# Performance work log

Measured on AMD Instinct MI355X. Metric: run time of the kernel, lower is better.

## Reference

```python
import jax, jax.numpy as jnp
import numpy as np

B, N = 8, 2048
IN_F, MID1, HID, MID2, OUT_F = 128, 128, 128, 128, 128
BIG = 9e15  # matches torch's 9000000000000000.0 additive mask constant


def _linear_params(key, out_d, in_d):
    # torch Linear layout: W is [out, in]
    kw, kb = jax.random.split(key)
    w = jax.random.normal(kw, (out_d, in_d), jnp.float32) * (1.0 / np.sqrt(in_d))
    b = jax.random.normal(kb, (out_d,), jnp.float32) * 0.01
    return w, b


def setup_inputs() -> dict:
    key = jax.random.key(0)
    ks = jax.random.split(key, 16)
    h = jax.random.normal(ks[0], (B, N, IN_F), jnp.float32)
    adj = jax.random.randint(ks[1], (B, N, N), 0, 2).astype(jnp.float32)
    vae2_fetures = jax.random.normal(ks[2], (B, N, OUT_F), jnp.float32)
    Wv1, bv1 = _linear_params(ks[3], MID1, IN_F)
    Wk1, bk1 = _linear_params(ks[4], MID1, IN_F)
    Wq1, bq1 = _linear_params(ks[5], MID1, IN_F)
    Wo1, bo1 = _linear_params(ks[6], HID, MID1)
    Wv2, bv2 = _linear_params(ks[7], MID2, HID)
    Wk2, bk2 = _linear_params(ks[8], MID2, HID)
    Wq2, bq2 = _linear_params(ks[9], MID2, HID)
    Wo2, bo2 = _linear_params(ks[10], OUT_F, MID2)
    Wf, bf = _linear_params(ks[11], OUT_F, 2 * OUT_F)
    return {
        "h": h, "adj": adj, "vae2_fetures": vae2_fetures,
        "Wv1": Wv1, "bv1": bv1, "Wk1": Wk1, "bk1": bk1, "Wq1": Wq1, "bq1": bq1,
        "Wo1": Wo1, "bo1": bo1,
        "Wv2": Wv2, "bv2": bv2, "Wk2": Wk2, "bk2": bk2, "Wq2": Wq2, "bq2": bq2,
        "Wo2": Wo2, "bo2": bo2, "Wf": Wf, "bf": bf,
    }


def _lin(x, W, b):
    return jnp.einsum('bnd,od->bno', x, W) + b


def _masked_att_block(x, adj, Wq, bq, Wk, bk, Wv, bv):
    v = jax.nn.relu(_lin(x, Wv, bv))          # [B,N,D]
    q = jax.nn.relu(_lin(x, Wq, bq))          # [B,N,D]
    k = jax.nn.relu(_lin(x, Wk, bk))          # [B,N,D]
    s = jnp.einsum('bnd,bmd->bnm', q, k)       # [B,N,N]
    masked = s * adj - BIG * (1.0 - adj)       # multiplicative + additive mask
    att = jax.nn.softmax(masked, axis=-1)
    return jnp.einsum('bnm,bmd->bnd', att, v)


def reference(h, adj, vae2_fetures,
              Wv1, bv1, Wk1, bk1, Wq1, bq1, Wo1, bo1,
              Wv2, bv2, Wk2, bk2, Wq2, bq2, Wo2, bo2,
              Wf, bf):
    f1 = _masked_att_block(h, adj, Wq1, bq1, Wk1, bk1, Wv1, bv1)
    f1 = _lin(f1, Wo1, bo1)                    # [B,N,HID]
    f2 = _masked_att_block(f1, adj, Wq2, bq2, Wk2, bk2, Wv2, bv2)
    f2 = _lin(f2, Wo2, bo2)                    # [B,N,OUT_F]
    f3 = jnp.concatenate([f2, vae2_fetures], axis=2)
    return _lin(f3, Wf, bf)                    # [B,N,OUT_F]
```

## Files before the change

kernel.cpp:

```cpp
#include <hip/hip_runtime.h>

typedef short s16x8 __attribute__((ext_vector_type(8)));
typedef float f32x4 __attribute__((ext_vector_type(4)));
typedef unsigned short u16x4v __attribute__((ext_vector_type(4)));

#define NSPLIT 4
#define NROWS 16384
#define MSHIFT 44.0f
#define NCH (2048 / NSPLIT / 64)

__device__ __forceinline__ unsigned short f2bf(float f) {
  union { float fl; unsigned int i; } v; v.fl = f;
  unsigned int x = v.i;
  x += 0x7fffu + ((x >> 16) & 1u);
  return (unsigned short)(x >> 16);
}
__device__ __forceinline__ s16x8 load8_bf16(const unsigned short* p) {
  return *(const s16x8*)p;
}
__device__ __forceinline__ s16x8 load8_f32(const float* p) {
  float4 a = *(const float4*)p;
  float4 b = *(const float4*)(p + 4);
  s16x8 r;
  r[0] = (short)f2bf(a.x); r[1] = (short)f2bf(a.y);
  r[2] = (short)f2bf(a.z); r[3] = (short)f2bf(a.w);
  r[4] = (short)f2bf(b.x); r[5] = (short)f2bf(b.y);
  r[6] = (short)f2bf(b.z); r[7] = (short)f2bf(b.w);
  return r;
}
__device__ __forceinline__ int vperm(int nn) {
  return (nn & ~31) | (((nn >> 2) & 3) << 3) | (((nn >> 4) & 1) << 2);
}

__device__ __forceinline__ void gload16(const void* g, void* l) {
  __builtin_amdgcn_global_load_lds(
      (const __attribute__((address_space(1))) void*)g,
      (__attribute__((address_space(3))) void*)l, 16, 0, 0);
}

__device__ __forceinline__ void pack_adj_body(
    const float* __restrict__ ADJ, unsigned long long* __restrict__ MASK,
    int pblk)
{
  const int t = threadIdx.x;
  const int w = t >> 6;
  const int lane = t & 63;
  const int row = pblk * 4 + w;

  const float4* src = (const float4*)(ADJ + (size_t)row * 2048);
  float4 v[8];
#pragma unroll
  for (int j = 0; j < 8; ++j) v[j] = src[j * 64 + lane];

  unsigned long long wm = 0ull;
#pragma unroll
  for (int j = 0; j < 8; ++j) {
    const unsigned long long b0 = __ballot(v[j].x != 0.f);
    wm = (lane == j * 4 + 0) ? b0 : wm;
    const unsigned long long b1 = __ballot(v[j].y != 0.f);
    wm = (lane == j * 4 + 1) ? b1 : wm;
    const unsigned long long b2 = __ballot(v[j].z != 0.f);
    wm = (lane == j * 4 + 2) ? b2 : wm;
    const unsigned long long b3 = __ballot(v[j].w != 0.f);
    wm = (lane == j * 4 + 3) ? b3 : wm;
  }

  if (lane < 32) MASK[(size_t)row * 32 + lane] = wm;
}

__device__ __forceinline__ void qkv_merged_body(
    const float* __restrict__ X,
    const float* __restrict__ Wq, const float* __restrict__ bq, unsigned short* __restrict__ oq,
    const float* __restrict__ Wk, const float* __restrict__ bk, unsigned short* __restrict__ ok,
    const float* __restrict__ Wv, const float* __restrict__ bv, unsigned short* __restrict__ ovt)
{
  const int t = threadIdx.x;
  const int w = t >> 6;
  const int lane = t & 63;
  const int l15 = lane & 15;
  const int quad = lane >> 4;
  const int mbase = blockIdx.x * 64;

  s16x8 af[4][4];
#pragma unroll
  for (int mt = 0; mt < 4; ++mt) {
    const float* ar = X + (size_t)(mbase + mt * 16 + l15) * 128;
#pragma unroll
    for (int ks = 0; ks < 4; ++ks) af[mt][ks] = load8_f32(ar + ks * 32 + quad * 8);
  }

  const float* Ws[3] = {Wq, Wk, Wv};
  const float* bs[3] = {bq, bk, bv};
  unsigned short* outs[3] = {oq, ok, ovt};

#pragma unroll
  for (int which = 0; which < 3; ++which) {
    const float* W = Ws[which];
    const float* bias = bs[which];
    unsigned short* out = outs[which];
#pragma unroll
    for (int nt = 0; nt < 2; ++nt) {
      const int n = (w * 2 + nt) * 16 + l15;
      const float* wr = W + (size_t)n * 128;
      s16x8 wf[4];
#pragma unroll
      for (int ks = 0; ks < 4; ++ks) wf[ks] = load8_f32(wr + ks * 32 + quad * 8);
      f32x4 acc[4];
#pragma unroll
      for (int mt = 0; mt < 4; ++mt) acc[mt] = (f32x4){0.f, 0.f, 0.f, 0.f};
#pragma unroll
      for (int mt = 0; mt < 4; ++mt)
#pragma unroll
        for (int ks = 0; ks < 4; ++ks)
          acc[mt] = __builtin_amdgcn_mfma_f32_16x16x32_bf16(af[mt][ks], wf[ks], acc[mt], 0, 0, 0);
      const float bv_ = bias[n];
      if (which < 2) {
#pragma unroll
        for (int mt = 0; mt < 4; ++mt)
#pragma unroll
          for (int r = 0; r < 4; ++r)
            out[(size_t)(mbase + mt * 16 + quad * 4 + r) * 128 + n] =
                f2bf(fmaxf(acc[mt][r] + bv_, 0.f));
      } else {
        const int b = mbase >> 11;
#pragma unroll
        for (int mt = 0; mt < 4; ++mt) {
          const int nn = (mbase & 2047) + mt * 16 + quad * 4;
          u16x4v pk;
#pragma unroll
          for (int r = 0; r < 4; ++r) pk[r] = f2bf(fmaxf(acc[mt][r] + bv_, 0.f));
          *(u16x4v*)(out + (size_t)(b * 128 + n) * 2048 + vperm(nn)) = pk;
        }
      }
    }
  }
}

__global__ __launch_bounds__(256) void qkv1_kernel(
    const float* __restrict__ x,
    const float* __restrict__ Wq, const float* __restrict__ bq, unsigned short* __restrict__ oq,
    const float* __restrict__ Wk, const float* __restrict__ bk, unsigned short* __restrict__ ok,
    const float* __restrict__ Wv, const float* __restrict__ bv, unsigned short* __restrict__ ovt,
    const float* __restrict__ adj, unsigned long long* __restrict__ mask)
{
  if (blockIdx.x < 256) qkv_merged_body(x, Wq, bq, oq, Wk, bk, ok, Wv, bv, ovt);
  else                  pack_adj_body(adj, mask, blockIdx.x - 256);
}

__global__ __launch_bounds__(256, 2) void attn_kernel(
    const unsigned short* __restrict__ Q,
    const unsigned short* __restrict__ K,
    const unsigned short* __restrict__ VT,
    const unsigned long long* __restrict__ MASK,
    float* __restrict__ pO, float* __restrict__ pl)
{
  __shared__ __align__(16) unsigned short kbuf[2][64][128];
  __shared__ __align__(16) unsigned short vbuf[2][128][64];

  const int t = threadIdx.x;
  const int w = t >> 6;
  const int lane = t & 63;
  const int l15 = lane & 15;
  const int quad = lane >> 4;
  const int x7 = l15 & 7;

  const int gq0 = blockIdx.x * 128;
  const int b   = gq0 >> 11;
  const int wq0 = (gq0 & 2047) + w * 32;
  const int kc0 = blockIdx.y * (2048 / NSPLIT);

  const unsigned short* Kb  = K  + (size_t)(b * 2048) * 128;
  const unsigned short* VTb = VT + (size_t)(b * 128) * 2048;
  const unsigned long long* Mb = MASK + (size_t)b * 2048 * 32;

  const int krow = t >> 4;
  const int kc16 = t & 15;
  const int kchunk = kc16 ^ (krow & 7);
  const int vrow = t >> 3;
  const int vc16 = t & 7;
  const int vchunk = vc16 ^ (vrow & 7);

  s16x8 qf[2][4];
#pragma unroll
  for (int mt = 0; mt < 2; ++mt) {
    const unsigned short* qrow = Q + (size_t)(gq0 + w * 32 + mt * 16 + l15) * 128;
#pragma unroll
    for (int ks = 0; ks < 4; ++ks) qf[mt][ks] = load8_bf16(qrow + ks * 32 + quad * 8);
  }

  s16x8 ones;
#pragma unroll
  for (int i = 0; i < 8; ++i) ones[i] = (short)0x3F80;

  f32x4 accO[2][8];
  f32x4 accL[2];
#pragma unroll
  for (int mt = 0; mt < 2; ++mt) {
    accL[mt] = (f32x4){0.f, 0.f, 0.f, 0.f};
#pragma unroll
    for (int dt = 0; dt < 8; ++dt) accO[mt][dt] = (f32x4){0.f, 0.f, 0.f, 0.f};
  }

#pragma unroll
  for (int i = 0; i < 4; ++i)
    gload16(Kb + (size_t)(kc0 + i * 16 + krow) * 128 + kchunk * 8,
            &kbuf[0][i * 16 + krow][kc16 * 8]);
#pragma unroll
  for (int i = 0; i < 4; ++i)
    gload16(VTb + (size_t)(i * 32 + vrow) * 2048 + kc0 + vchunk * 8,
            &vbuf[0][i * 32 + vrow][vc16 * 8]);

  __syncthreads();

  for (int g = 0; g < 2; ++g) {
    const int jj = (kc0 >> 8) + g;
    ulonglong2 m01[2], m23[2];
#pragma unroll
    for (int mt = 0; mt < 2; ++mt) {
      const unsigned long long* mrow = Mb + (size_t)(wq0 + mt * 16 + l15) * 32 + jj * 4;
      m01[mt] = *(const ulonglong2*)mrow;
      m23[mt] = *(const ulonglong2*)(mrow + 2);
    }

#pragma unroll
    for (int cg = 0; cg < 4; ++cg) {
      const int kc = kc0 + g * 256 + cg * 64;
      unsigned short (*kb)[128] = kbuf[cg & 1];
      unsigned short (*vb)[64]  = vbuf[cg & 1];

      if (g == 0 || cg < 3) {
        unsigned short (*kbn)[128] = kbuf[(cg + 1) & 1];
        unsigned short (*vbn)[64]  = vbuf[(cg + 1) & 1];
#pragma unroll
        for (int i = 0; i < 4; ++i)
          gload16(Kb + (size_t)(kc + 64 + i * 16 + krow) * 128 + kchunk * 8,
                  &kbn[i * 16 + krow][kc16 * 8]);
#pragma unroll
        for (int i = 0; i < 4; ++i)
          gload16(VTb + (size_t)(i * 32 + vrow) * 2048 + (kc + 64) + vchunk * 8,
                  &vbn[i * 32 + vrow][vc16 * 8]);
      }

      f32x4 sv[2][4];
#pragma unroll
      for (int nt = 0; nt < 4; ++nt) {
        sv[0][nt] = (f32x4){0.f, 0.f, 0.f, 0.f};
        sv[1][nt] = (f32x4){0.f, 0.f, 0.f, 0.f};
      }
      __builtin_amdgcn_s_setprio(1);
#pragma unroll
      for (int nt = 0; nt < 4; ++nt)
#pragma unroll
        for (int ks = 0; ks < 4; ++ks) {
          s16x8 kf = *(const s16x8*)&kb[nt * 16 + l15][((ks * 4 + quad) ^ x7) * 8];
          sv[0][nt] = __builtin_amdgcn_mfma_f32_16x16x32_bf16(kf, qf[0][ks], sv[0][nt], 0, 0, 0);
          sv[1][nt] = __builtin_amdgcn_mfma_f32_16x16x32_bf16(kf, qf[1][ks], sv[1][nt], 0, 0, 0);
        }
      __builtin_amdgcn_s_setprio(0);

      s16x8 pf[2][2];
#pragma unroll
      for (int mt = 0; mt < 2; ++mt) {
        const unsigned long long bse0 = m01[mt].x >> (cg * 16 + quad);
        const unsigned long long bse1 = m01[mt].y >> (cg * 16 + quad);
        const unsigned long long bse2 = m23[mt].x >> (cg * 16 + quad);
        const unsigned long long bse3 = m23[mt].y >> (cg * 16 + quad);
#pragma unroll
        for (int ks = 0; ks < 2; ++ks) {
          s16x8 v;
#pragma unroll
          for (int half = 0; half < 2; ++half) {
            const int nt = ks * 2 + half;
#pragma unroll
            for (int r = 0; r < 4; ++r) {
              const float e = __expf(sv[mt][nt][r] - MSHIFT);
              const unsigned long long bw = (r == 0) ? bse0 : (r == 1) ? bse1
                                          : (r == 2) ? bse2 : bse3;
              const bool keep = (bw >> (nt * 4)) & 1ull;
              v[half * 4 + r] = (short)f2bf(keep ? e : 0.f);
            }
          }
          pf[mt][ks] = v;
        }
      }

      __builtin_amdgcn_s_setprio(1);
#pragma unroll
      for (int mt = 0; mt < 2; ++mt)
#pragma unroll
        for (int ks = 0; ks < 2; ++ks)
          accL[mt] = __builtin_amdgcn_mfma_f32_16x16x32_bf16(ones, pf[mt][ks], accL[mt], 0, 0, 0);

#pragma unroll
      for (int dt = 0; dt < 8; ++dt)
#pragma unroll
        for (int ks = 0; ks < 2; ++ks) {
          s16x8 vf = *(const s16x8*)&vb[dt * 16 + l15][((ks * 4 + quad) ^ x7) * 8];
          accO[0][dt] = __builtin_amdgcn_mfma_f32_16x16x32_bf16(vf, pf[0][ks], accO[0][dt], 0, 0, 0);
          accO[1][dt] = __builtin_amdgcn_mfma_f32_16x16x32_bf16(vf, pf[1][ks], accO[1][dt], 0, 0, 0);
        }
      __builtin_amdgcn_s_setprio(0);

      __syncthreads();
    }
  }

  float* pOs = pO + (size_t)blockIdx.y * NROWS * 128;
#pragma unroll
  for (int mt = 0; mt < 2; ++mt) {
    const int qg = gq0 + w * 32 + mt * 16 + l15;
#pragma unroll
    for (int dt = 0; dt < 8; ++dt)
      *(f32x4*)(pOs + (size_t)qg * 128 + dt * 16 + quad * 4) = accO[mt][dt];
  }
  if (quad == 0) {
#pragma unroll
    for (int mt = 0; mt < 2; ++mt)
      pl[blockIdx.y * NROWS + gq0 + w * 32 + mt * 16 + l15] = accL[mt][0];
  }
}

__device__ __forceinline__ void combine64(
    const float* __restrict__ pO, const float* __restrict__ pl, int grow0,
    unsigned short (*At)[136])
{
  const int t = threadIdx.x;
#pragma unroll
  for (int u = 0; u < 4; ++u) {
    const int unit = u * 256 + t;
    const int row = unit >> 4;
    const int col8 = (unit & 15) * 8;
    const int grow = grow0 + row;
    float lsum = 0.f;
#pragma unroll
    for (int s = 0; s < NSPLIT; ++s) lsum += pl[s * NROWS + grow];
    const float inv = (lsum > 0.f) ? 1.f / lsum : 0.f;
    float acc8[8];
#pragma unroll
    for (int i = 0; i < 8; ++i) acc8[i] = 0.f;
#pragma unroll
    for (int s = 0; s < NSPLIT; ++s) {
      const float* p = pO + (size_t)s * NROWS * 128 + (size_t)grow * 128 + col8;
      float4 x0 = *(const float4*)p;
      float4 x1 = *(const float4*)(p + 4);
      acc8[0] += x0.x; acc8[1] += x0.y; acc8[2] += x0.z; acc8[3] += x0.w;
      acc8[4] += x1.x; acc8[5] += x1.y; acc8[6] += x1.z; acc8[7] += x1.w;
    }
#pragma unroll
    for (int i = 0; i < 8; ++i) At[row][col8 + i] = f2bf(acc8[i] * inv);
  }
}

__global__ __launch_bounds__(256) void redqkv_kernel(
    const float* __restrict__ pO, const float* __restrict__ pl,
    const float* __restrict__ Wo, const float* __restrict__ bo,
    const float* __restrict__ Wq, const float* __restrict__ bq, unsigned short* __restrict__ oq,
    const float* __restrict__ Wk, const float* __restrict__ bk, unsigned short* __restrict__ ok,
    const float* __restrict__ Wv, const float* __restrict__ bv, unsigned short* __restrict__ ovt)
{
  __shared__ __align__(16) unsigned short At[64][136];
  __shared__ __align__(16) unsigned short Bt[64][136];
  const int t = threadIdx.x;
  const int grow0 = blockIdx.x * 64;

  combine64(pO, pl, grow0, At);
  __syncthreads();

  const int w = t >> 6;
  const int lane = t & 63;
  const int l15 = lane & 15;
  const int quad = lane >> 4;

  s16x8 af[4][4];
#pragma unroll
  for (int mt = 0; mt < 4; ++mt)
#pragma unroll
    for (int ks = 0; ks < 4; ++ks)
      af[mt][ks] = *(const s16x8*)&At[mt * 16 + l15][ks * 32 + quad * 8];

#pragma unroll
  for (int nt = 0; nt < 2; ++nt) {
    const int n = (w * 2 + nt) * 16 + l15;
    const float* wr = Wo + (size_t)n * 128;
    s16x8 wf[4];
#pragma unroll
    for (int ks = 0; ks < 4; ++ks) wf[ks] = load8_f32(wr + ks * 32 + quad * 8);
    f32x4 acc[4];
#pragma unroll
    for (int mt = 0; mt < 4; ++mt) acc[mt] = (f32x4){0.f, 0.f, 0.f, 0.f};
#pragma unroll
    for (int mt = 0; mt < 4; ++mt)
#pragma unroll
      for (int ks = 0; ks < 4; ++ks)
        acc[mt] = __builtin_amdgcn_mfma_f32_16x16x32_bf16(af[mt][ks], wf[ks], acc[mt], 0, 0, 0);
    const float bv_ = bo[n];
#pragma unroll
    for (int mt = 0; mt < 4; ++mt)
#pragma unroll
      for (int r = 0; r < 4; ++r)
        Bt[mt * 16 + quad * 4 + r][n] = f2bf(acc[mt][r] + bv_);
  }
  __syncthreads();

  s16x8 a2[4][4];
#pragma unroll
  for (int mt = 0; mt < 4; ++mt)
#pragma unroll
    for (int ks = 0; ks < 4; ++ks)
      a2[mt][ks] = *(const s16x8*)&Bt[mt * 16 + l15][ks * 32 + quad * 8];

#pragma unroll
  for (int which = 0; which < 3; ++which) {
    const float* W = (which == 0) ? Wq : (which == 1) ? Wk : Wv;
    const float* bb = (which == 0) ? bq : (which == 1) ? bk : bv;
    unsigned short* out = (which == 0) ? oq : (which == 1) ? ok : ovt;
#pragma unroll
    for (int nt = 0; nt < 2; ++nt) {
      const int n = (w * 2 + nt) * 16 + l15;
      const float* wr = W + (size_t)n * 128;
      s16x8 wf[4];
#pragma unroll
      for (int ks = 0; ks < 4; ++ks) wf[ks] = load8_f32(wr + ks * 32 + quad * 8);
      f32x4 acc[4];
#pragma unroll
      for (int mt = 0; mt < 4; ++mt) acc[mt] = (f32x4){0.f, 0.f, 0.f, 0.f};
#pragma unroll
      for (int mt = 0; mt < 4; ++mt)
#pragma unroll
        for (int ks = 0; ks < 4; ++ks)
          acc[mt] = __builtin_amdgcn_mfma_f32_16x16x32_bf16(a2[mt][ks], wf[ks], acc[mt], 0, 0, 0);
      const float bv_ = bb[n];
      if (which < 2) {
#pragma unroll
        for (int mt = 0; mt < 4; ++mt)
#pragma unroll
          for (int r = 0; r < 4; ++r)
            out[(size_t)(grow0 + mt * 16 + quad * 4 + r) * 128 + n] =
                f2bf(fmaxf(acc[mt][r] + bv_, 0.f));
      } else {
        const int b = grow0 >> 11;
#pragma unroll
        for (int mt = 0; mt < 4; ++mt) {
          const int nn = (grow0 & 2047) + mt * 16 + quad * 4;
          u16x4v pk;
#pragma unroll
          for (int r = 0; r < 4; ++r) pk[r] = f2bf(fmaxf(acc[mt][r] + bv_, 0.f));
          *(u16x4v*)(out + (size_t)(b * 128 + n) * 2048 + vperm(nn)) = pk;
        }
      }
    }
  }
}

__global__ __launch_bounds__(256) void redfinal_kernel(
    const float* __restrict__ pO, const float* __restrict__ pl,
    const float* __restrict__ Wo, const float* __restrict__ bo,
    const float* __restrict__ Wf, const float* __restrict__ bff,
    const float* __restrict__ vae2, float* __restrict__ out)
{
  __shared__ __align__(16) unsigned short At[64][136];
  __shared__ __align__(16) unsigned short Bt[64][136];
  const int t = threadIdx.x;
  const int grow0 = blockIdx.x * 64;

  combine64(pO, pl, grow0, At);
  __syncthreads();

  const int w = t >> 6;
  const int lane = t & 63;
  const int l15 = lane & 15;
  const int quad = lane >> 4;

  s16x8 af[4][4];
#pragma unroll
  for (int mt = 0; mt < 4; ++mt)
#pragma unroll
    for (int ks = 0; ks < 4; ++ks)
      af[mt][ks] = *(const s16x8*)&At[mt * 16 + l15][ks * 32 + quad * 8];

#pragma unroll
  for (int nt = 0; nt < 2; ++nt) {
    const int n = (w * 2 + nt) * 16 + l15;
    const float* wr = Wo + (size_t)n * 128;
    s16x8 wf[4];
#pragma unroll
    for (int ks = 0; ks < 4; ++ks) wf[ks] = load8_f32(wr + ks * 32 + quad * 8);
    f32x4 acc[4];
#pragma unroll
    for (int mt = 0; mt < 4; ++mt) acc[mt] = (f32x4){0.f, 0.f, 0.f, 0.f};
#pragma unroll
    for (int mt = 0; mt < 4; ++mt)
#pragma unroll
      for (int ks = 0; ks < 4; ++ks)
        acc[mt] = __builtin_amdgcn_mfma_f32_16x16x32_bf16(af[mt][ks], wf[ks], acc[mt], 0, 0, 0);
    const float bv_ = bo[n];
#pragma unroll
    for (int mt = 0; mt < 4; ++mt)
#pragma unroll
      for (int r = 0; r < 4; ++r)
        Bt[mt * 16 + quad * 4 + r][n] = f2bf(acc[mt][r] + bv_);
  }
  __syncthreads();

  s16x8 a1[4][4], a2[4][4];
#pragma unroll
  for (int mt = 0; mt < 4; ++mt) {
#pragma unroll
    for (int ks = 0; ks < 4; ++ks)
      a1[mt][ks] = *(const s16x8*)&Bt[mt * 16 + l15][ks * 32 + quad * 8];
    const float* vrow = vae2 + (size_t)(grow0 + mt * 16 + l15) * 128;
#pragma unroll
    for (int ks = 0; ks < 4; ++ks) a2[mt][ks] = load8_f32(vrow + ks * 32 + quad * 8);
  }

#pragma unroll
  for (int nt = 0; nt < 2; ++nt) {
    const int n = (w * 2 + nt) * 16 + l15;
    const float* wr = Wf + (size_t)n * 256;
    s16x8 wfl[4], wfr[4];
#pragma unroll
    for (int ks = 0; ks < 4; ++ks) {
      wfl[ks] = load8_f32(wr + ks * 32 + quad * 8);
      wfr[ks] = load8_f32(wr + 128 + ks * 32 + quad * 8);
    }
    f32x4 acc[4];
#pragma unroll
    for (int mt = 0; mt < 4; ++mt) acc[mt] = (f32x4){0.f, 0.f, 0.f, 0.f};
#pragma unroll
    for (int mt = 0; mt < 4; ++mt) {
#pragma unroll
      for (int ks = 0; ks < 4; ++ks)
        acc[mt] = __builtin_amdgcn_mfma_f32_16x16x32_bf16(a1[mt][ks], wfl[ks], acc[mt], 0, 0, 0);
#pragma unroll
      for (int ks = 0; ks < 4; ++ks)
        acc[mt] = __builtin_amdgcn_mfma_f32_16x16x32_bf16(a2[mt][ks], wfr[ks], acc[mt], 0, 0, 0);
    }
    const float bv_ = bff[n];
#pragma unroll
    for (int mt = 0; mt < 4; ++mt)
#pragma unroll
      for (int r = 0; r < 4; ++r)
        out[(size_t)(grow0 + mt * 16 + quad * 4 + r) * 128 + n] = acc[mt][r] + bv_;
  }
}

extern "C" void kernel_launch(void* const* d_in, const int* in_sizes, int n_in,
                              void* d_out, int out_size, void* d_ws, size_t ws_size,
                              hipStream_t stream)
{
  const float* h    = (const float*)d_in[0];
  const float* adj  = (const float*)d_in[1];
  const float* vae2 = (const float*)d_in[2];
  const float* Wv1  = (const float*)d_in[3];
  const float* bv1  = (const float*)d_in[4];
  const float* Wk1  = (const float*)d_in[5];
  const float* bk1  = (const float*)d_in[6];
  const float* Wq1  = (const float*)d_in[7];
  const float* bq1  = (const float*)d_in[8];
  const float* Wo1  = (const float*)d_in[9];
  const float* bo1  = (const float*)d_in[10];
  const float* Wv2  = (const float*)d_in[11];
  const float* bv2  = (const float*)d_in[12];
  const float* Wk2  = (const float*)d_in[13];
  const float* bk2  = (const float*)d_in[14];
  const float* Wq2  = (const float*)d_in[15];
  const float* bq2  = (const float*)d_in[16];
  const float* Wo2  = (const float*)d_in[17];
  const float* bo2  = (const float*)d_in[18];
  const float* Wf   = (const float*)d_in[19];
  const float* bff  = (const float*)d_in[20];

  char* wsb = (char*)d_ws;
  const size_t MB = 1u << 20;
  unsigned short* s_q  = (unsigned short*)(wsb + 0 * MB);
  unsigned short* s_k  = (unsigned short*)(wsb + 4 * MB);
  unsigned short* s_vt = (unsigned short*)(wsb + 8 * MB);
  unsigned long long* maskp = (unsigned long long*)(wsb + 12 * MB);
  float* pO = (float*)(wsb + 16 * MB);
  float* pl = (float*)(wsb + 48 * MB);

  qkv1_kernel<<<dim3(256 + 4096), dim3(256), 0, stream>>>(
      h, Wq1, bq1, s_q, Wk1, bk1, s_k, Wv1, bv1, s_vt, adj, maskp);
  attn_kernel<<<dim3(128, NSPLIT), dim3(256), 0, stream>>>(
      s_q, s_k, s_vt, maskp, pO, pl);
  redqkv_kernel<<<dim3(256), dim3(256), 0, stream>>>(
      pO, pl, Wo1, bo1, Wq2, bq2, s_q, Wk2, bk2, s_k, Wv2, bv2, s_vt);
  attn_kernel<<<dim3(128, NSPLIT), dim3(256), 0, stream>>>(
      s_q, s_k, s_vt, maskp, pO, pl);
  redfinal_kernel<<<dim3(256), dim3(256), 0, stream>>>(
      pO, pl, Wo2, bo2, Wf, bff, vae2, (float*)d_out);
}
```

Measured before the change: 355.0 us.

## Fuse all stages into one cooperative persistent kernel with grid syncs

Replaces the five separate launches with a single cooperative kernel of 256 blocks of 512 threads. It uses grid-wide barriers between the QKV/mask-pack, attention, reduce+QKV, attention and final stages, and falls back to separate 512-thread kernels if the cooperative launch fails. Block work is re-tiled to 512 threads: each warp now handles one 16-column slice, attention covers 256 query rows per block, and mask packing does 64 rows per block. The aim is to remove launch gaps and tail effects between kernels. In exchange, grid.sync costs are added, occupancy is fixed by the cooperative launch, and a per-process static flag caches whether cooperative launch is supported.

```diff
diff --git a/kernel.cpp b/kernel.cpp
--- a/kernel.cpp
+++ b/kernel.cpp
@@ -1,4 +1,7 @@
 #include <hip/hip_runtime.h>
+#include <hip/hip_cooperative_groups.h>
+
+namespace cg = cooperative_groups;
 
 typedef short s16x8 __attribute__((ext_vector_type(8)));
 typedef float f32x4 __attribute__((ext_vector_type(4)));
@@ -7,7 +10,6 @@
 #define NSPLIT 4
 #define NROWS 16384
 #define MSHIFT 44.0f
-#define NCH (2048 / NSPLIT / 64)
 
 __device__ __forceinline__ unsigned short f2bf(float f) {
   union { float fl; unsigned int i; } v; v.fl = f;
@@ -38,48 +40,51 @@
       (__attribute__((address_space(3))) void*)l, 16, 0, 0);
 }
 
-__device__ __forceinline__ void pack_adj_body(
+__device__ __forceinline__ void pack64_body(
     const float* __restrict__ ADJ, unsigned long long* __restrict__ MASK,
-    int pblk)
+    int bid)
 {
   const int t = threadIdx.x;
   const int w = t >> 6;
   const int lane = t & 63;
-  const int row = pblk * 4 + w;
-
-  const float4* src = (const float4*)(ADJ + (size_t)row * 2048);
-  float4 v[8];
-#pragma unroll
-  for (int j = 0; j < 8; ++j) v[j] = src[j * 64 + lane];
-
-  unsigned long long wm = 0ull;
-#pragma unroll
-  for (int j = 0; j < 8; ++j) {
-    const unsigned long long b0 = __ballot(v[j].x != 0.f);
-    wm = (lane == j * 4 + 0) ? b0 : wm;
-    const unsigned long long b1 = __ballot(v[j].y != 0.f);
-    wm = (lane == j * 4 + 1) ? b1 : wm;
-    const unsigned long long b2 = __ballot(v[j].z != 0.f);
-    wm = (lane == j * 4 + 2) ? b2 : wm;
-    const unsigned long long b3 = __ballot(v[j].w != 0.f);
-    wm = (lane == j * 4 + 3) ? b3 : wm;
-  }
-
-  if (lane < 32) MASK[(size_t)row * 32 + lane] = wm;
-}
-
-__device__ __forceinline__ void qkv_merged_body(
+  const int row0 = bid * 64 + w * 8;
+
+  for (int i = 0; i < 8; ++i) {
+    const int row = row0 + i;
+    const float4* src = (const float4*)(ADJ + (size_t)row * 2048);
+    float4 v[8];
+#pragma unroll
+    for (int j = 0; j < 8; ++j) v[j] = src[j * 64 + lane];
+
+    unsigned long long wm = 0ull;
+#pragma unroll
+    for (int j = 0; j < 8; ++j) {
+      const unsigned long long b0 = __ballot(v[j].x != 0.f);
+      wm = (lane == j * 4 + 0) ? b0 : wm;
+      const unsigned long long b1 = __ballot(v[j].y != 0.f);
+      wm = (lane == j * 4 + 1) ? b1 : wm;
+      const unsigned long long b2 = __ballot(v[j].z != 0.f);
+      wm = (lane == j * 4 + 2) ? b2 : wm;
+      const unsigned long long b3 = __ballot(v[j].w != 0.f);
+      wm = (lane == j * 4 + 3) ? b3 : wm;
+    }
+    if (lane < 32) MASK[(size_t)row * 32 + lane] = wm;
+  }
+}
+
+__device__ __forceinline__ void qkv64_body(
     const float* __restrict__ X,
     const float* __restrict__ Wq, const float* __restrict__ bq, unsigned short* __restrict__ oq,
     const float* __restrict__ Wk, const float* __restrict__ bk, unsigned short* __restrict__ ok,
-    const float* __restrict__ Wv, const float* __restrict__ bv, unsigned short* __restrict__ ovt)
+    const float* __restrict__ Wv, const float* __restrict__ bv, unsigned short* __restrict__ ovt,
+    int bid)
 {
   const int t = threadIdx.x;
   const int w = t >> 6;
   const int lane = t & 63;
   const int l15 = lane & 15;
   const int quad = lane >> 4;
-  const int mbase = blockIdx.x * 64;
+  const int mbase = bid * 64;
 
   s16x8 af[4][4];
 #pragma unroll
@@ -92,71 +97,54 @@
   const float* Ws[3] = {Wq, Wk, Wv};
   const float* bs[3] = {bq, bk, bv};
   unsigned short* outs[3] = {oq, ok, ovt};
+  const int n = w * 16 + l15;
 
 #pragma unroll
   for (int which = 0; which < 3; ++which) {
-    const float* W = Ws[which];
-    const float* bias = bs[which];
+    const float* wr = Ws[which] + (size_t)n * 128;
+    s16x8 wf[4];
+#pragma unroll
+    for (int ks = 0; ks < 4; ++ks) wf[ks] = load8_f32(wr + ks * 32 + quad * 8);
+    f32x4 acc[4];
+#pragma unroll
+    for (int mt = 0; mt < 4; ++mt) acc[mt] = (f32x4){0.f, 0.f, 0.f, 0.f};
+#pragma unroll
+    for (int mt = 0; mt < 4; ++mt)
+#pragma unroll
+      for (int ks = 0; ks < 4; ++ks)
+        acc[mt] = __builtin_amdgcn_mfma_f32_16x16x32_bf16(af[mt][ks], wf[ks], acc[mt], 0, 0, 0);
+    const float bv_ = bs[which][n];
     unsigned short* out = outs[which];
-#pragma unroll
-    for (int nt = 0; nt < 2; ++nt) {
-      const int n = (w * 2 + nt) * 16 + l15;
-      const float* wr = W + (size_t)n * 128;
-      s16x8 wf[4];
-#pragma unroll
-      for (int ks = 0; ks < 4; ++ks) wf[ks] = load8_f32(wr + ks * 32 + quad * 8);
-      f32x4 acc[4];
-#pragma unroll
-      for (int mt = 0; mt < 4; ++mt) acc[mt] = (f32x4){0.f, 0.f, 0.f, 0.f};
+    if (which < 2) {
 #pragma unroll
       for (int mt = 0; mt < 4; ++mt)
 #pragma unroll
-        for (int ks = 0; ks < 4; ++ks)
-          acc[mt] = __builtin_amdgcn_mfma_f32_16x16x32_bf16(af[mt][ks], wf[ks], acc[mt], 0, 0, 0);
-      const float bv_ = bias[n];
-      if (which < 2) {
-#pragma unroll
-        for (int mt = 0; mt < 4; ++mt)
-#pragma unroll
-          for (int r = 0; r < 4; ++r)
-            out[(size_t)(mbase + mt * 16 + quad * 4 + r) * 128 + n] =
-                f2bf(fmaxf(acc[mt][r] + bv_, 0.f));
-      } else {
-        const int b = mbase >> 11;
-#pragma unroll
-        for (int mt = 0; mt < 4; ++mt) {
-          const int nn = (mbase & 2047) + mt * 16 + quad * 4;
-          u16x4v pk;
-#pragma unroll
-          for (int r = 0; r < 4; ++r) pk[r] = f2bf(fmaxf(acc[mt][r] + bv_, 0.f));
-          *(u16x4v*)(out + (size_t)(b * 128 + n) * 2048 + vperm(nn)) = pk;
-        }
+        for (int r = 0; r < 4; ++r)
+          out[(size_t)(mbase + mt * 16 + quad * 4 + r) * 128 + n] =
+              f2bf(fmaxf(acc[mt][r] + bv_, 0.f));
+    } else {
+      const int b = mbase >> 11;
+#pragma unroll
+      for (int mt = 0; mt < 4; ++mt) {
+        const int nn = (mbase & 2047) + mt * 16 + quad * 4;
+        u16x4v pk;
+#pragma unroll
+        for (int r = 0; r < 4; ++r) pk[r] = f2bf(fmaxf(acc[mt][r] + bv_, 0.f));
+        *(u16x4v*)(out + (size_t)(b * 128 + n) * 2048 + vperm(nn)) = pk;
       }
     }
   }
 }
 
-__global__ __launch_bounds__(256) void qkv1_kernel(
-    const float* __restrict__ x,
-    const float* __restrict__ Wq, const float* __restrict__ bq, unsigned short* __restrict__ oq,
-    const float* __restrict__ Wk, const float* __restrict__ bk, unsigned short* __restrict__ ok,
-    const float* __restrict__ Wv, const float* __restrict__ bv, unsigned short* __restrict__ ovt,
-    const float* __restrict__ adj, unsigned long long* __restrict__ mask)
-{
-  if (blockIdx.x < 256) qkv_merged_body(x, Wq, bq, oq, Wk, bk, ok, Wv, bv, ovt);
-  else                  pack_adj_body(adj, mask, blockIdx.x - 256);
-}
-
-__global__ __launch_bounds__(256, 2) void attn_kernel(
+__device__ __forceinline__ void attn_body(
     const unsigned short* __restrict__ Q,
     const unsigned short* __restrict__ K,
     const unsigned short* __restrict__ VT,
     const unsigned long long* __restrict__ MASK,
-    float* __restrict__ pO, float* __restrict__ pl)
-{
-  __shared__ __align__(16) unsigned short kbuf[2][64][128];
-  __shared__ __align__(16) unsigned short vbuf[2][128][64];
-
+    float* __restrict__ pO, float* __restrict__ pl,
+    unsigned short (*kbuf)[64][128], unsigned short (*vbuf)[128][64],
+    int qb, int sp)
+{
   const int t = threadIdx.x;
   const int w = t >> 6;
   const int lane = t & 63;
@@ -164,21 +152,17 @@
   const int quad = lane >> 4;
   const int x7 = l15 & 7;
 
-  const int gq0 = blockIdx.x * 128;
+  const int gq0 = qb * 256;
   const int b   = gq0 >> 11;
   const int wq0 = (gq0 & 2047) + w * 32;
-  const int kc0 = blockIdx.y * (2048 / NSPLIT);
+  const int kc0 = sp * (2048 / NSPLIT);
 
   const unsigned short* Kb  = K  + (size_t)(b * 2048) * 128;
   const unsigned short* VTb = VT + (size_t)(b * 128) * 2048;
   const unsigned long long* Mb = MASK + (size_t)b * 2048 * 32;
 
-  const int krow = t >> 4;
-  const int kc16 = t & 15;
-  const int kchunk = kc16 ^ (krow & 7);
-  const int vrow = t >> 3;
-  const int vc16 = t & 7;
-  const int vchunk = vc16 ^ (vrow & 7);
+  const int kchunk = (t & 15) ^ ((t >> 4) & 7);
+  const int vchunk = (t & 7) ^ ((t >> 3) & 7);
 
   s16x8 qf[2][4];
 #pragma unroll
@@ -202,13 +186,17 @@
   }
 
 #pragma unroll
-  for (int i = 0; i < 4; ++i)
-    gload16(Kb + (size_t)(kc0 + i * 16 + krow) * 128 + kchunk * 8,
-            &kbuf[0][i * 16 + krow][kc16 * 8]);
-#pragma unroll
-  for (int i = 0; i < 4; ++i)
-    gload16(VTb + (size_t)(i * 32 + vrow) * 2048 + kc0 + vchunk * 8,
-            &vbuf[0][i * 32 + vrow][vc16 * 8]);
+  for (int i = 0; i < 2; ++i) {
+    const int slot = i * 512 + t;
+    gload16(Kb + (size_t)(kc0 + (slot >> 4)) * 128 + kchunk * 8,
+            &kbuf[0][slot >> 4][(slot & 15) * 8]);
+  }
+#pragma unroll
+  for (int i = 0; i < 2; ++i) {
+    const int slot = i * 512 + t;
+    gload16(VTb + (size_t)(slot >> 3) * 2048 + kc0 + vchunk * 8,
+            &vbuf[0][slot >> 3][(slot & 7) * 8]);
+  }
 
   __syncthreads();
 
@@ -223,22 +211,26 @@
     }
 
 #pragma unroll
-    for (int cg = 0; cg < 4; ++cg) {
-      const int kc = kc0 + g * 256 + cg * 64;
-      unsigned short (*kb)[128] = kbuf[cg & 1];
-      unsigned short (*vb)[64]  = vbuf[cg & 1];
-
-      if (g == 0 || cg < 3) {
-        unsigned short (*kbn)[128] = kbuf[(cg + 1) & 1];
-        unsigned short (*vbn)[64]  = vbuf[(cg + 1) & 1];
-#pragma unroll
-        for (int i = 0; i < 4; ++i)
-          gload16(Kb + (size_t)(kc + 64 + i * 16 + krow) * 128 + kchunk * 8,
-                  &kbn[i * 16 + krow][kc16 * 8]);
-#pragma unroll
-        for (int i = 0; i < 4; ++i)
-          gload16(VTb + (size_t)(i * 32 + vrow) * 2048 + (kc + 64) + vchunk * 8,
-                  &vbn[i * 32 + vrow][vc16 * 8]);
+    for (int cgi = 0; cgi < 4; ++cgi) {
+      const int kc = kc0 + g * 256 + cgi * 64;
+      unsigned short (*kb)[128] = kbuf[cgi & 1];
+      unsigned short (*vb)[64]  = vbuf[cgi & 1];
+
+      if (g == 0 || cgi < 3) {
+        unsigned short (*kbn)[128] = kbuf[(cgi + 1) & 1];
+        unsigned short (*vbn)[64]  = vbuf[(cgi + 1) & 1];
+#pragma unroll
+        for (int i = 0; i < 2; ++i) {
+          const int slot = i * 512 + t;
+          gload16(Kb + (size_t)(kc + 64 + (slot >> 4)) * 128 + kchunk * 8,
+                  &kbn[slot >> 4][(slot & 15) * 8]);
+        }
+#pragma unroll
+        for (int i = 0; i < 2; ++i) {
+          const int slot = i * 512 + t;
+          gload16(VTb + (size_t)(slot >> 3) * 2048 + (kc + 64) + vchunk * 8,
+                  &vbn[slot >> 3][(slot & 7) * 8]);
+        }
       }
 
       f32x4 sv[2][4];
@@ -261,10 +253,10 @@
       s16x8 pf[2][2];
 #pragma unroll
       for (int mt = 0; mt < 2; ++mt) {
-        const unsigned long long bse0 = m01[mt].x >> (cg * 16 + quad);
-        const unsigned long long bse1 = m01[mt].y >> (cg * 16 + quad);
-        const unsigned long long bse2 = m23[mt].x >> (cg * 16 + quad);
-        const unsigned long long bse3 = m23[mt].y >> (cg * 16 + quad);
+        const unsigned long long bse0 = m01[mt].x >> (cgi * 16 + quad);
+        const unsigned long long bse1 = m01[mt].y >> (cgi * 16 + quad);
+        const unsigned long long bse2 = m23[mt].x >> (cgi * 16 + quad);
+        const unsigned long long bse3 = m23[mt].y >> (cgi * 16 + quad);
 #pragma unroll
         for (int ks = 0; ks < 2; ++ks) {
           s16x8 v;
@@ -305,7 +297,7 @@
     }
   }
 
-  float* pOs = pO + (size_t)blockIdx.y * NROWS * 128;
+  float* pOs = pO + (size_t)sp * NROWS * 128;
 #pragma unroll
   for (int mt = 0; mt < 2; ++mt) {
     const int qg = gq0 + w * 32 + mt * 16 + l15;
@@ -316,7 +308,7 @@
   if (quad == 0) {
 #pragma unroll
     for (int mt = 0; mt < 2; ++mt)
-      pl[blockIdx.y * NROWS + gq0 + w * 32 + mt * 16 + l15] = accL[mt][0];
+      pl[sp * NROWS + gq0 + w * 32 + mt * 16 + l15] = accL[mt][0];
   }
 }
 
@@ -326,8 +318,8 @@
 {
   const int t = threadIdx.x;
 #pragma unroll
-  for (int u = 0; u < 4; ++u) {
-    const int unit = u * 256 + t;
+  for (int u = 0; u < 2; ++u) {
+    const int unit = u * 512 + t;
     const int row = unit >> 4;
     const int col8 = (unit & 15) * 8;
     const int grow = grow0 + row;
@@ -351,7 +343,254 @@
   }
 }
 
-__global__ __launch_bounds__(256) void redqkv_kernel(
+__device__ __forceinline__ void redqkv64_body(
+    const float* __restrict__ pO, const float* __restrict__ pl,
+    const float* __restrict__ Wo, const float* __restrict__ bo,
+    const float* __restrict__ Wq, const float* __restrict__ bq, unsigned short* __restrict__ oq,
+    const float* __restrict__ Wk, const float* __restrict__ bk, unsigned short* __restrict__ ok,
+    const float* __restrict__ Wv, const float* __restrict__ bv, unsigned short* __restrict__ ovt,
+    unsigned short (*At)[136], unsigned short (*Bt)[136], int bid)
+{
+  const int t = threadIdx.x;
+  const int grow0 = bid * 64;
+
+  combine64(pO, pl, grow0, At);
+  __syncthreads();
+
+  const int w = t >> 6;
+  const int lane = t & 63;
+  const int l15 = lane & 15;
+  const int quad = lane >> 4;
+  const int n = w * 16 + l15;
+
+  s16x8 af[4][4];
+#pragma unroll
+  for (int mt = 0; mt < 4; ++mt)
+#pragma unroll
+    for (int ks = 0; ks < 4; ++ks)
+      af[mt][ks] = *(const s16x8*)&At[mt * 16 + l15][ks * 32 + quad * 8];
+
+  {
+    const float* wr = Wo + (size_t)n * 128;
+    s16x8 wf[4];
+#pragma unroll
+    for (int ks = 0; ks < 4; ++ks) wf[ks] = load8_f32(wr + ks * 32 + quad * 8);
+    f32x4 acc[4];
+#pragma unroll
+    for (int mt = 0; mt < 4; ++mt) acc[mt] = (f32x4){0.f, 0.f, 0.f, 0.f};
+#pragma unroll
+    for (int mt = 0; mt < 4; ++mt)
+#pragma unroll
+      for (int ks = 0; ks < 4; ++ks)
+        acc[mt] = __builtin_amdgcn_mfma_f32_16x16x32_bf16(af[mt][ks], wf[ks], acc[mt], 0, 0, 0);
+    const float bv_ = bo[n];
+#pragma unroll
+    for (int mt = 0; mt < 4; ++mt)
+#pragma unroll
+      for (int r = 0; r < 4; ++r)
+        Bt[mt * 16 + quad * 4 + r][n] = f2bf(acc[mt][r] + bv_);
+  }
+  __syncthreads();
+
+  s16x8 a2[4][4];
+#pragma unroll
+  for (int mt = 0; mt < 4; ++mt)
+#pragma unroll
+    for (int ks = 0; ks < 4; ++ks)
+      a2[mt][ks] = *(const s16x8*)&Bt[mt * 16 + l15][ks * 32 + quad * 8];
+
+#pragma unroll
+  for (int which = 0; which < 3; ++which) {
+    const float* W = (which == 0) ? Wq : (which == 1) ? Wk : Wv;
+    const float* bb = (which == 0) ? bq : (which == 1) ? bk : bv;
+    unsigned short* out = (which == 0) ? oq : (which == 1) ? ok : ovt;
+    const float* wr = W + (size_t)n * 128;
+    s16x8 wf[4];
+#pragma unroll
+    for (int ks = 0; ks < 4; ++ks) wf[ks] = load8_f32(wr + ks * 32 + quad * 8);
+    f32x4 acc[4];
+#pragma unroll
+    for (int mt = 0; mt < 4; ++mt) acc[mt] = (f32x4){0.f, 0.f, 0.f, 0.f};
+#pragma unroll
+    for (int mt = 0; mt < 4; ++mt)
+#pragma unroll
+      for (int ks = 0; ks < 4; ++ks)
+        acc[mt] = __builtin_amdgcn_mfma_f32_16x16x32_bf16(a2[mt][ks], wf[ks], acc[mt], 0, 0, 0);
+    const float bv_ = bb[n];
+    if (which < 2) {
+#pragma unroll
+      for (int mt = 0; mt < 4; ++mt)
+#pragma unroll
+        for (int r = 0; r < 4; ++r)
+          out[(size_t)(grow0 + mt * 16 + quad * 4 + r) * 128 + n] =
+              f2bf(fmaxf(acc[mt][r] + bv_, 0.f));
+    } else {
+      const int b = grow0 >> 11;
+#pragma unroll
+      for (int mt = 0; mt < 4; ++mt) {
+        const int nn = (grow0 & 2047) + mt * 16 + quad * 4;
+        u16x4v pk;
+#pragma unroll
+        for (int r = 0; r < 4; ++r) pk[r] = f2bf(fmaxf(acc[mt][r] + bv_, 0.f));
+        *(u16x4v*)(out + (size_t)(b * 128 + n) * 2048 + vperm(nn)) = pk;
+      }
+    }
+  }
+}
+
+__device__ __forceinline__ void redfinal64_body(
+    const float* __restrict__ pO, const float* __restrict__ pl,
+    const float* __restrict__ Wo, const float* __restrict__ bo,
+    const float* __restrict__ Wf, const float* __restrict__ bff,
+    const float* __restrict__ vae2, float* __restrict__ out,
+    unsigned short (*At)[136], unsigned short (*Bt)[136], int bid)
+{
+  const int t = threadIdx.x;
+  const int grow0 = bid * 64;
+
+  combine64(pO, pl, grow0, At);
+  __syncthreads();
+
+  const int w = t >> 6;
+  const int lane = t & 63;
+  const int l15 = lane & 15;
+  const int quad = lane >> 4;
+  const int n = w * 16 + l15;
+
+  s16x8 af[4][4];
+#pragma unroll
+  for (int mt = 0; mt < 4; ++mt)
+#pragma unroll
+    for (int ks = 0; ks < 4; ++ks)
+      af[mt][ks] = *(const s16x8*)&At[mt * 16 + l15][ks * 32 + quad * 8];
+
+  {
+    const float* wr = Wo + (size_t)n * 128;
+    s16x8 wf[4];
+#pragma unroll
+    for (int ks = 0; ks < 4; ++ks) wf[ks] = load8_f32(wr + ks * 32 + quad * 8);
+    f32x4 acc[4];
+#pragma unroll
+    for (int mt = 0; mt < 4; ++mt) acc[mt] = (f32x4){0.f, 0.f, 0.f, 0.f};
+#pragma unroll
+    for (int mt = 0; mt < 4; ++mt)
+#pragma unroll
+      for (int ks = 0; ks < 4; ++ks)
+        acc[mt] = __builtin_amdgcn_mfma_f32_16x16x32_bf16(af[mt][ks], wf[ks], acc[mt], 0, 0, 0);
+    const float bv_ = bo[n];
+#pragma unroll
+    for (int mt = 0; mt < 4; ++mt)
+#pragma unroll
+      for (int r = 0; r < 4; ++r)
+        Bt[mt * 16 + quad * 4 + r][n] = f2bf(acc[mt][r] + bv_);
+  }
+  __syncthreads();
+
+  s16x8 a1[4][4], a2[4][4];
+#pragma unroll
+  for (int mt = 0; mt < 4; ++mt) {
+#pragma unroll
+    for (int ks = 0; ks < 4; ++ks)
+      a1[mt][ks] = *(const s16x8*)&Bt[mt * 16 + l15][ks * 32 + quad * 8];
+    const float* vrow = vae2 + (size_t)(grow0 + mt * 16 + l15) * 128;
+#pragma unroll
+    for (int ks = 0; ks < 4; ++ks) a2[mt][ks] = load8_f32(vrow + ks * 32 + quad * 8);
+  }
+
+  {
+    const float* wr = Wf + (size_t)n * 256;
+    s16x8 wfl[4], wfr[4];
+#pragma unroll
+    for (int ks = 0; ks < 4; ++ks) {
+      wfl[ks] = load8_f32(wr + ks * 32 + quad * 8);
+      wfr[ks] = load8_f32(wr + 128 + ks * 32 + quad * 8);
+    }
+    f32x4 acc[4];
+#pragma unroll
+    for (int mt = 0; mt < 4; ++mt) acc[mt] = (f32x4){0.f, 0.f, 0.f, 0.f};
+#pragma unroll
+    for (int mt = 0; mt < 4; ++mt) {
+#pragma unroll
+      for (int ks = 0; ks < 4; ++ks)
+        acc[mt] = __builtin_amdgcn_mfma_f32_16x16x32_bf16(a1[mt][ks], wfl[ks], acc[mt], 0, 0, 0);
+#pragma unroll
+      for (int ks = 0; ks < 4; ++ks)
+        acc[mt] = __builtin_amdgcn_mfma_f32_16x16x32_bf16(a2[mt][ks], wfr[ks], acc[mt], 0, 0, 0);
+    }
+    const float bv_ = bff[n];
+#pragma unroll
+    for (int mt = 0; mt < 4; ++mt)
+#pragma unroll
+      for (int r = 0; r < 4; ++r)
+        out[(size_t)(grow0 + mt * 16 + quad * 4 + r) * 128 + n] = acc[mt][r] + bv_;
+  }
+}
+
+__global__ __launch_bounds__(512, 2) void fused_kernel(
+    const float* __restrict__ x, const float* __restrict__ adj, const float* __restrict__ vae2,
+    const float* __restrict__ Wq1, const float* __restrict__ bq1,
+    const float* __restrict__ Wk1, const float* __restrict__ bk1,
+    const float* __restrict__ Wv1, const float* __restrict__ bv1,
+    const float* __restrict__ Wo1, const float* __restrict__ bo1,
+    const float* __restrict__ Wq2, const float* __restrict__ bq2,
+    const float* __restrict__ Wk2, const float* __restrict__ bk2,
+    const float* __restrict__ Wv2, const float* __restrict__ bv2,
+    const float* __restrict__ Wo2, const float* __restrict__ bo2,
+    const float* __restrict__ Wf, const float* __restrict__ bff,
+    unsigned short* __restrict__ s_q, unsigned short* __restrict__ s_k,
+    unsigned short* __restrict__ s_vt, unsigned long long* __restrict__ maskp,
+    float* __restrict__ pO, float* __restrict__ pl, float* __restrict__ out)
+{
+  __shared__ __align__(16) unsigned char smem[65536];
+  unsigned short (*kbuf)[64][128] = (unsigned short (*)[64][128])smem;
+  unsigned short (*vbuf)[128][64] = (unsigned short (*)[128][64])(smem + 32768);
+  unsigned short (*At)[136] = (unsigned short (*)[136])smem;
+  unsigned short (*Bt)[136] = (unsigned short (*)[136])(smem + 32768);
+
+  const int bid = blockIdx.x;
+  const int qb = bid & 63;
+  const int sp = bid >> 6;
+  cg::grid_group grid = cg::this_grid();
+
+  qkv64_body(x, Wq1, bq1, s_q, Wk1, bk1, s_k, Wv1, bv1, s_vt, bid);
+  pack64_body(adj, maskp, bid);
+  __threadfence(); grid.sync();
+
+  attn_body(s_q, s_k, s_vt, maskp, pO, pl, kbuf, vbuf, qb, sp);
+  __threadfence(); grid.sync();
+
+  redqkv64_body(pO, pl, Wo1, bo1, Wq2, bq2, s_q, Wk2, bk2, s_k, Wv2, bv2, s_vt,
+                At, Bt, bid);
+  __threadfence(); grid.sync();
+
+  attn_body(s_q, s_k, s_vt, maskp, pO, pl, kbuf, vbuf, qb, sp);
+  __threadfence(); grid.sync();
+
+  redfinal64_body(pO, pl, Wo2, bo2, Wf, bff, vae2, out, At, Bt, bid);
+}
+
+__global__ __launch_bounds__(512, 2) void p0_kernel(
+    const float* __restrict__ x,
+    const float* __restrict__ Wq, const float* __restrict__ bq, unsigned short* __restrict__ oq,
+    const float* __restrict__ Wk, const float* __restrict__ bk, unsigned short* __restrict__ ok,
+    const float* __restrict__ Wv, const float* __restrict__ bv, unsigned short* __restrict__ ovt,
+    const float* __restrict__ adj, unsigned long long* __restrict__ mask)
+{
+  qkv64_body(x, Wq, bq, oq, Wk, bk, ok, Wv, bv, ovt, blockIdx.x);
+  pack64_body(adj, mask, blockIdx.x);
+}
+
+__global__ __launch_bounds__(512, 2) void attn_sep_kernel(
+    const unsigned short* __restrict__ Q, const unsigned short* __restrict__ K,
+    const unsigned short* __restrict__ VT, const unsigned long long* __restrict__ MASK,
+    float* __restrict__ pO, float* __restrict__ pl)
+{
+  __shared__ __align__(16) unsigned short kbuf[2][64][128];
+  __shared__ __align__(16) unsigned short vbuf[2][128][64];
+  attn_body(Q, K, VT, MASK, pO, pl, kbuf, vbuf, blockIdx.x & 63, blockIdx.x >> 6);
+}
+
+__global__ __launch_bounds__(512, 2) void redqkv_sep_kernel(
     const float* __restrict__ pO, const float* __restrict__ pl,
     const float* __restrict__ Wo, const float* __restrict__ bo,
     const float* __restrict__ Wq, const float* __restrict__ bq, unsigned short* __restrict__ oq,
@@ -360,99 +599,10 @@
 {
   __shared__ __align__(16) unsigned short At[64][136];
   __shared__ __align__(16) unsigned short Bt[64][136];
-  const int t = threadIdx.x;
-  const int grow0 = blockIdx.x * 64;
-
-  combine64(pO, pl, grow0, At);
-  __syncthreads();
-
-  const int w = t >> 6;
-  const int lane = t & 63;
-  const int l15 = lane & 15;
-  const int quad = lane >> 4;
-
-  s16x8 af[4][4];
-#pragma unroll
-  for (int mt = 0; mt < 4; ++mt)
-#pragma unroll
-    for (int ks = 0; ks < 4; ++ks)
-      af[mt][ks] = *(const s16x8*)&At[mt * 16 + l15][ks * 32 + quad * 8];
-
-#pragma unroll
-  for (int nt = 0; nt < 2; ++nt) {
-    const int n = (w * 2 + nt) * 16 + l15;
-    const float* wr = Wo + (size_t)n * 128;
-    s16x8 wf[4];
-#pragma unroll
-    for (int ks = 0; ks < 4; ++ks) wf[ks] = load8_f32(wr + ks * 32 + quad * 8);
-    f32x4 acc[4];
-#pragma unroll
-    for (int mt = 0; mt < 4; ++mt) acc[mt] = (f32x4){0.f, 0.f, 0.f, 0.f};
-#pragma unroll
-    for (int mt = 0; mt < 4; ++mt)
-#pragma unroll
-      for (int ks = 0; ks < 4; ++ks)
-        acc[mt] = __builtin_amdgcn_mfma_f32_16x16x32_bf16(af[mt][ks], wf[ks], acc[mt], 0, 0, 0);
-    const float bv_ = bo[n];
-#pragma unroll
-    for (int mt = 0; mt < 4; ++mt)
-#pragma unroll
-      for (int r = 0; r < 4; ++r)
-        Bt[mt * 16 + quad * 4 + r][n] = f2bf(acc[mt][r] + bv_);
-  }
-  __syncthreads();
-
-  s16x8 a2[4][4];
-#pragma unroll
-  for (int mt = 0; mt < 4; ++mt)
-#pragma unroll
-    for (int ks = 0; ks < 4; ++ks)
-      a2[mt][ks] = *(const s16x8*)&Bt[mt * 16 + l15][ks * 32 + quad * 8];
-
-#pragma unroll
-  for (int which = 0; which < 3; ++which) {
-    const float* W = (which == 0) ? Wq : (which == 1) ? Wk : Wv;
-    const float* bb = (which == 0) ? bq : (which == 1) ? bk : bv;
-    unsigned short* out = (which == 0) ? oq : (which == 1) ? ok : ovt;
-#pragma unroll
-    for (int nt = 0; nt < 2; ++nt) {
-      const int n = (w * 2 + nt) * 16 + l15;
-      const float* wr = W + (size_t)n * 128;
-      s16x8 wf[4];
-#pragma unroll
-      for (int ks = 0; ks < 4; ++ks) wf[ks] = load8_f32(wr + ks * 32 + quad * 8);
-      f32x4 acc[4];
-#pragma unroll
-      for (int mt = 0; mt < 4; ++mt) acc[mt] = (f32x4){0.f, 0.f, 0.f, 0.f};
-#pragma unroll
-      for (int mt = 0; mt < 4; ++mt)
-#pragma unroll
-        for (int ks = 0; ks < 4; ++ks)
-          acc[mt] = __builtin_amdgcn_mfma_f32_16x16x32_bf16(a2[mt][ks], wf[ks], acc[mt], 0, 0, 0);
-      const float bv_ = bb[n];
-      if (which < 2) {
-#pragma unroll
-        for (int mt = 0; mt < 4; ++mt)
-#pragma unroll
-          for (int r = 0; r < 4; ++r)
-            out[(size_t)(grow0 + mt * 16 + quad * 4 + r) * 128 + n] =
-                f2bf(fmaxf(acc[mt][r] + bv_, 0.f));
-      } else {
-        const int b = grow0 >> 11;
-#pragma unroll
-        for (int mt = 0; mt < 4; ++mt) {
-          const int nn = (grow0 & 2047) + mt * 16 + quad * 4;
-          u16x4v pk;
-#pragma unroll
-          for (int r = 0; r < 4; ++r) pk[r] = f2bf(fmaxf(acc[mt][r] + bv_, 0.f));
-          *(u16x4v*)(out + (size_t)(b * 128 + n) * 2048 + vperm(nn)) = pk;
-        }
-      }
-    }
-  }
-}
-
-__global__ __launch_bounds__(256) void redfinal_kernel(
+  redqkv64_body(pO, pl, Wo, bo, Wq, bq, oq, Wk, bk, ok, Wv, bv, ovt, At, Bt, blockIdx.x);
+}
+
+__global__ __launch_bounds__(512, 2) void redfinal_sep_kernel(
     const float* __restrict__ pO, const float* __restrict__ pl,
     const float* __restrict__ Wo, const float* __restrict__ bo,
     const float* __restrict__ Wf, const float* __restrict__ bff,
@@ -460,88 +610,7 @@
 {
   __shared__ __align__(16) unsigned short At[64][136];
   __shared__ __align__(16) unsigned short Bt[64][136];
-  const int t = threadIdx.x;
-  const int grow0 = blockIdx.x * 64;
-
-  combine64(pO, pl, grow0, At);
-  __syncthreads();
-
-  const int w = t >> 6;
-  const int lane = t & 63;
-  const int l15 = lane & 15;
-  const int quad = lane >> 4;
-
-  s16x8 af[4][4];
-#pragma unroll
-  for (int mt = 0; mt < 4; ++mt)
-#pragma unroll
-    for (int ks = 0; ks < 4; ++ks)
-      af[mt][ks] = *(const s16x8*)&At[mt * 16 + l15][ks * 32 + quad * 8];
-
-#pragma unroll
-  for (int nt = 0; nt < 2; ++nt) {
-    const int n = (w * 2 + nt) * 16 + l15;
-    const float* wr = Wo + (size_t)n * 128;
-    s16x8 wf[4];
-#pragma unroll
-    for (int ks = 0; ks < 4; ++ks) wf[ks] = load8_f32(wr + ks * 32 + quad * 8);
-    f32x4 acc[4];
-#pragma unroll
-    for (int mt = 0; mt < 4; ++mt) acc[mt] = (f32x4){0.f, 0.f, 0.f, 0.f};
-#pragma unroll
-    for (int mt = 0; mt < 4; ++mt)
-#pragma unroll
-      for (int ks = 0; ks < 4; ++ks)
-        acc[mt] = __builtin_amdgcn_mfma_f32_16x16x32_bf16(af[mt][ks], wf[ks], acc[mt], 0, 0, 0);
-    const float bv_ = bo[n];
-#pragma unroll
-    for (int mt = 0; mt < 4; ++mt)
-#pragma unroll
-      for (int r = 0; r < 4; ++r)
-        Bt[mt * 16 + quad * 4 + r][n] = f2bf(acc[mt][r] + bv_);
-  }
-  __syncthreads();
-
-  s16x8 a1[4][4], a2[4][4];
-#pragma unroll
-  for (int mt = 0; mt < 4; ++mt) {
-#pragma unroll
-    for (int ks = 0; ks < 4; ++ks)
-      a1[mt][ks] = *(const s16x8*)&Bt[mt * 16 + l15][ks * 32 + quad * 8];
-    const float* vrow = vae2 + (size_t)(grow0 + mt * 16 + l15) * 128;
-#pragma unroll
-    for (int ks = 0; ks < 4; ++ks) a2[mt][ks] = load8_f32(vrow + ks * 32 + quad * 8);
-  }
-
-#pragma unroll
-  for (int nt = 0; nt < 2; ++nt) {
-    const int n = (w * 2 + nt) * 16 + l15;
-    const float* wr = Wf + (size_t)n * 256;
-    s16x8 wfl[4], wfr[4];
-#pragma unroll
-    for (int ks = 0; ks < 4; ++ks) {
-      wfl[ks] = load8_f32(wr + ks * 32 + quad * 8);
-      wfr[ks] = load8_f32(wr + 128 + ks * 32 + quad * 8);
-    }
-    f32x4 acc[4];
-#pragma unroll
-    for (int mt = 0; mt < 4; ++mt) acc[mt] = (f32x4){0.f, 0.f, 0.f, 0.f};
-#pragma unroll
-    for (int mt = 0; mt < 4; ++mt) {
-#pragma unroll
-      for (int ks = 0; ks < 4; ++ks)
-        acc[mt] = __builtin_amdgcn_mfma_f32_16x16x32_bf16(a1[mt][ks], wfl[ks], acc[mt], 0, 0, 0);
-#pragma unroll
-      for (int ks = 0; ks < 4; ++ks)
-        acc[mt] = __builtin_amdgcn_mfma_f32_16x16x32_bf16(a2[mt][ks], wfr[ks], acc[mt], 0, 0, 0);
-    }
-    const float bv_ = bff[n];
-#pragma unroll
-    for (int mt = 0; mt < 4; ++mt)
-#pragma unroll
-      for (int r = 0; r < 4; ++r)
-        out[(size_t)(grow0 + mt * 16 + quad * 4 + r) * 128 + n] = acc[mt][r] + bv_;
-  }
+  redfinal64_body(pO, pl, Wo, bo, Wf, bff, vae2, out, At, Bt, blockIdx.x);
 }
 
 extern "C" void kernel_launch(void* const* d_in, const int* in_sizes, int n_in,
@@ -578,15 +647,33 @@
   unsigned long long* maskp = (unsigned long long*)(wsb + 12 * MB);
   float* pO = (float*)(wsb + 16 * MB);
   float* pl = (float*)(wsb + 48 * MB);
-
-  qkv1_kernel<<<dim3(256 + 4096), dim3(256), 0, stream>>>(
+  float* outp = (float*)d_out;
+
+  static int coop_ok = -1;
+  if (coop_ok != 0) {
+    void* args[] = {
+        (void*)&h, (void*)&adj, (void*)&vae2,
+        (void*)&Wq1, (void*)&bq1, (void*)&Wk1, (void*)&bk1, (void*)&Wv1, (void*)&bv1,
+        (void*)&Wo1, (void*)&bo1,
+        (void*)&Wq2, (void*)&bq2, (void*)&Wk2, (void*)&bk2, (void*)&Wv2, (void*)&bv2,
+        (void*)&Wo2, (void*)&bo2,
+        (void*)&Wf, (void*)&bff,
+        (void*)&s_q, (void*)&s_k, (void*)&s_vt, (void*)&maskp,
+        (void*)&pO, (void*)&pl, (void*)&outp};
+    hipError_t e = hipLaunchCooperativeKernel((const void*)fused_kernel,
+                                              dim3(256), dim3(512), args, 0, stream);
+    if (coop_ok < 0) coop_ok = (e == hipSuccess) ? 1 : 0;
+    if (coop_ok == 1) return;
+  }
+
+  p0_kernel<<<dim3(256), dim3(512), 0, stream>>>(
       h, Wq1, bq1, s_q, Wk1, bk1, s_k, Wv1, bv1, s_vt, adj, maskp);
-  attn_kernel<<<dim3(128, NSPLIT), dim3(256), 0, stream>>>(
+  attn_sep_kernel<<<dim3(256), dim3(512), 0, stream>>>(
       s_q, s_k, s_vt, maskp, pO, pl);
-  redqkv_kernel<<<dim3(256), dim3(256), 0, stream>>>(
+  redqkv_sep_kernel<<<dim3(256), dim3(512), 0, stream>>>(
       pO, pl, Wo1, bo1, Wq2, bq2, s_q, Wk2, bk2, s_k, Wv2, bv2, s_vt);
-  attn_kernel<<<dim3(128, NSPLIT), dim3(256), 0, stream>>>(
+  attn_sep_kernel<<<dim3(256), dim3(512), 0, stream>>>(
       s_q, s_k, s_vt, maskp, pO, pl);
-  redfinal_kernel<<<dim3(256), dim3(256), 0, stream>>>(
+  redfinal_sep_kernel<<<dim3(256), dim3(512), 0, stream>>>(
       pO, pl, Wo2, bo2, Wf, bff, vae2, (float*)d_out);
 }
```

After: 816.3 us. 130% more time.
